# Optimization experiments

Measured on AMD Instinct MI355X. Metric: run time of the kernel, lower is better.

The kernel has to match this reference:

```python
import jax, jax.numpy as jnp
import numpy as np

N = 50000
E = 1600000
AUG = 6
IN = 128
HEADS = 8
HID = 16
OUT = 40


def setup_inputs() -> dict:
    key = jax.random.key(0)
    ks = jax.random.split(key, 14)
    s = 0.1
    return {
        "x": jax.random.normal(ks[0], (N, IN + AUG), jnp.float32),
        "edge_index": jax.random.randint(ks[1], (2, E), 0, N, jnp.int32),
        "mlp_w1": jax.random.normal(ks[2], (AUG, 16), jnp.float32) * s,
        "mlp_b1": jnp.zeros((16,), jnp.float32),
        "mlp_w2": jax.random.normal(ks[3], (16, 1), jnp.float32) * s,
        "mlp_b2": jnp.zeros((1,), jnp.float32),
        "w1": jax.random.normal(ks[4], (IN, HEADS * HID), jnp.float32) * s,
        "att_src1": jax.random.normal(ks[5], (HEADS, HID), jnp.float32) * s,
        "att_dst1": jax.random.normal(ks[6], (HEADS, HID), jnp.float32) * s,
        "bias1": jnp.zeros((HEADS * HID,), jnp.float32),
        "w2": jax.random.normal(ks[7], (HEADS * HID, OUT), jnp.float32) * s,
        "att_src2": jax.random.normal(ks[8], (1, OUT), jnp.float32) * s,
        "att_dst2": jax.random.normal(ks[9], (1, OUT), jnp.float32) * s,
        "bias2": jnp.zeros((OUT,), jnp.float32),
    }


def _gat_conv(x, src, dst, W, att_src, att_dst, bias, concat):
    # PyG GATConv (eval mode): linear -> per-edge leaky_relu attention ->
    # softmax over incoming edges per destination -> weighted scatter-sum.
    n = x.shape[0]
    heads, ch = att_src.shape
    h = (x @ W).reshape(n, heads, ch)                # [N,H,C]
    a_src = (h * att_src[None]).sum(-1)              # [N,H]
    a_dst = (h * att_dst[None]).sum(-1)              # [N,H]
    e = jax.nn.leaky_relu(a_src[src] + a_dst[dst], 0.2)  # [E,H]
    emax = jax.ops.segment_max(e, dst, num_segments=n)   # self-loops ensure nonempty
    p = jnp.exp(e - emax[dst])
    denom = jax.ops.segment_sum(p, dst, num_segments=n)
    alpha = p / denom[dst]                           # [E,H]
    msg = h[src] * alpha[:, :, None]                 # [E,H,C]
    out = jax.ops.segment_sum(msg, dst, num_segments=n)  # [N,H,C]
    out = out.reshape(n, heads * ch) if concat else out.mean(axis=1)
    return out + bias


def reference(x, edge_index, mlp_w1, mlp_b1, mlp_w2, mlp_b2,
              w1, att_src1, att_dst1, bias1, w2, att_src2, att_dst2, bias2):
    n = x.shape[0]
    orig = x[:, :-AUG]
    aug = x[:, -AUG:]
    aug = (aug - aug.mean(axis=0)) / jnp.std(aug, axis=0, ddof=1)  # torch std is unbiased
    scale = jax.nn.sigmoid(jax.nn.relu(aug @ mlp_w1 + mlp_b1) @ mlp_w2 + mlp_b2)  # [N,1]
    h = orig * (1.0 + scale)
    # dropout is identity in eval mode
    loops = jnp.arange(n, dtype=edge_index.dtype)
    src = jnp.concatenate([edge_index[0], loops])
    dst = jnp.concatenate([edge_index[1], loops])
    h = jax.nn.relu(_gat_conv(h, src, dst, w1, att_src1, att_dst1, bias1, True))
    out = _gat_conv(h, src, dst, w2, att_src2, att_dst2, bias2, False)
    return jax.nn.log_softmax(out, axis=1)
```

## Files before the change

kernel.cpp:

```cpp
#include <hip/hip_runtime.h>
#include <hip/hip_fp16.h>

#define XDIM 134
#define FEAT 128
#define AUGN 6
#define NH 8
#define HD 16
#define OUTD 40
#define PS 132
#define SB 256
#define PB 256
#define MAXNB 256
#define G8S 64
#define WTS 130
#define DST 132
#define W2C 48
#define DST2 52

typedef float v2f __attribute__((ext_vector_type(2)));
typedef _Float16 h8t __attribute__((ext_vector_type(8)));
typedef float f32x4 __attribute__((ext_vector_type(4)));

__device__ __forceinline__ float rlf(float v, int lane) {
  return __int_as_float(__builtin_amdgcn_readlane(__float_as_int(v), lane));
}

__global__ __launch_bounds__(256) void k_stats1(const float* __restrict__ x,
                                                float* __restrict__ part,
                                                int N) {
  __shared__ float red[4][12];
  float s[AUGN] = {0, 0, 0, 0, 0, 0}, q[AUGN] = {0, 0, 0, 0, 0, 0};
  for (int n = blockIdx.x * blockDim.x + threadIdx.x; n < N;
       n += gridDim.x * blockDim.x) {
    const float* r = x + (size_t)n * XDIM + FEAT;
    float2 v0 = *(const float2*)r;
    float2 v1 = *(const float2*)(r + 2);
    float2 v2 = *(const float2*)(r + 4);
    float v[AUGN] = {v0.x, v0.y, v1.x, v1.y, v2.x, v2.y};
#pragma unroll
    for (int i = 0; i < AUGN; i++) {
      s[i] += v[i];
      q[i] += v[i] * v[i];
    }
  }
#pragma unroll
  for (int i = 0; i < AUGN; i++) {
    for (int m = 1; m < 64; m <<= 1) {
      s[i] += __shfl_xor(s[i], m);
      q[i] += __shfl_xor(q[i], m);
    }
  }
  int wv = threadIdx.x >> 6, l = threadIdx.x & 63;
  if (l == 0) {
#pragma unroll
    for (int i = 0; i < AUGN; i++) {
      red[wv][i] = s[i];
      red[wv][6 + i] = q[i];
    }
  }
  __syncthreads();
  int t = threadIdx.x;
  if (t < 12) {
    part[blockIdx.x * 12 + t] =
        red[0][t] + red[1][t] + red[2][t] + red[3][t];
  }
}

__global__ __launch_bounds__(256) void k_scale(
    const float* __restrict__ x, const float* __restrict__ part,
    const float* __restrict__ w1, const float* __restrict__ b1,
    const float* __restrict__ w2, const float* __restrict__ b2,
    float* __restrict__ scl, int N) {
  __shared__ float red[4][12];
  __shared__ float sred[12];
  int t = threadIdx.x;
  {
    float v[12];
#pragma unroll
    for (int c = 0; c < 12; c++) v[c] = part[t * 12 + c];
#pragma unroll
    for (int c = 0; c < 12; c++)
      for (int m = 1; m < 64; m <<= 1) v[c] += __shfl_xor(v[c], m);
    int wv = t >> 6, l = t & 63;
    if (l == 0) {
#pragma unroll
      for (int c = 0; c < 12; c++) red[wv][c] = v[c];
    }
    __syncthreads();
    if (t < 12) sred[t] = red[0][t] + red[1][t] + red[2][t] + red[3][t];
    __syncthreads();
  }
  int n = blockIdx.x * 256 + t;
  if (n >= N) return;
  const float* r = x + (size_t)n * XDIM + FEAT;
  float a[AUGN];
  float invN = 1.0f / (float)N;
#pragma unroll
  for (int i = 0; i < AUGN; i++) {
    float sum = sred[i], sq = sred[6 + i];
    float mean = sum * invN;
    float var = (sq - sum * mean) / (float)(N - 1);
    a[i] = (r[i] - mean) / sqrtf(var);
  }
  float s2 = b2[0];
#pragma unroll
  for (int j = 0; j < 16; j++) {
    float z = b1[j];
#pragma unroll
    for (int i = 0; i < AUGN; i++) z = fmaf(a[i], w1[i * 16 + j], z);
    z = fmaxf(z, 0.0f);
    s2 = fmaf(z, w2[j], s2);
  }
  float sig = 1.0f / (1.0f + __expf(-s2));
  scl[n] = 1.0f + sig;
}

__global__ __launch_bounds__(256) void k_bh(const int* __restrict__ ei,
                                            int* __restrict__ cnt, int E,
                                            int NB) {
  __shared__ int hist[MAXNB];
  int t = threadIdx.x;
  for (int b = t; b < NB; b += 256) hist[b] = 0;
  __syncthreads();
  int ch = (E + PB - 1) / PB;
  int lo = blockIdx.x * ch, hi = min(lo + ch, E);
  for (int e = lo + t; e < hi; e += 256)
    atomicAdd(&hist[ei[E + e] >> 8], 1);
  __syncthreads();
  for (int b = t; b < NB; b += 256)
    cnt[(size_t)b * PB + blockIdx.x] = hist[b];
}

__global__ __launch_bounds__(256) void k_sc1(int* __restrict__ cnt,
                                             int* __restrict__ bsum) {
  __shared__ int ps[256];
  int b = blockIdx.x, t = threadIdx.x;
  int v = cnt[(size_t)b * PB + t];
  ps[t] = v;
  __syncthreads();
  for (int d = 1; d < 256; d <<= 1) {
    int u = (t >= d) ? ps[t - d] : 0;
    __syncthreads();
    ps[t] += u;
    __syncthreads();
  }
  cnt[(size_t)b * PB + t] = ps[t] - v;
  if (t == 255) bsum[b] = ps[255];
}

__global__ __launch_bounds__(256) void k_part(const int* __restrict__ ei,
                                              const int* __restrict__ cnt,
                                              const int* __restrict__ bsum,
                                              int* __restrict__ ebuf, int E,
                                              int NB) {
  __shared__ int bex[MAXNB];
  __shared__ int cur[MAXNB];
  int t = threadIdx.x;
  int v = (t < NB) ? bsum[t] : 0;
  bex[t] = v;
  __syncthreads();
  for (int d = 1; d < 256; d <<= 1) {
    int u = (t >= d) ? bex[t - d] : 0;
    __syncthreads();
    bex[t] += u;
    __syncthreads();
  }
  if (t < NB) cur[t] = (bex[t] - v) + cnt[(size_t)t * PB + blockIdx.x];
  __syncthreads();
  int ch = (E + PB - 1) / PB;
  int lo = blockIdx.x * ch, hi = min(lo + ch, E);
  for (int e = lo + t; e < hi; e += 256) {
    int s = ei[e], d = ei[E + e];
    int pos = atomicAdd(&cur[d >> 8], 1);
    ebuf[pos] = (s << 8) | (d & 255);
  }
}

__global__ __launch_bounds__(256) void k_bcsr(const int* __restrict__ ebuf,
                                              const int* __restrict__ bsum,
                                              int* __restrict__ offs,
                                              int* __restrict__ csr, int N,
                                              int E, int NB) {
  __shared__ int bex[MAXNB];
  __shared__ int dl[256];
  __shared__ int sc[256];
  __shared__ int cu[256];
  int b = blockIdx.x, t = threadIdx.x;
  {
    int v = (t < NB) ? bsum[t] : 0;
    bex[t] = v;
    __syncthreads();
    for (int d = 1; d < 256; d <<= 1) {
      int u = (t >= d) ? bex[t - d] : 0;
      __syncthreads();
      bex[t] += u;
      __syncthreads();
    }
    int incl = bex[t];
    __syncthreads();
    bex[t] = incl - v;
    __syncthreads();
  }
  int nn = min(256, N - b * 256);
  int rs = bex[b];
  int re = (b + 1 < NB) ? bex[b + 1] : E;
  int csrbase = rs + b * 256;
  dl[t] = 0;
  __syncthreads();
  for (int j = rs + t; j < re; j += 256)
    atomicAdd(&dl[ebuf[j] & 255], 1);
  __syncthreads();
  int v = (t < nn) ? dl[t] + 1 : 0;
  sc[t] = v;
  __syncthreads();
  for (int d = 1; d < 256; d <<= 1) {
    int u = (t >= d) ? sc[t - d] : 0;
    __syncthreads();
    sc[t] += u;
    __syncthreads();
  }
  int excl = sc[t] - v;
  if (t < nn) {
    int node = b * 256 + t;
    offs[node] = csrbase + excl;
    csr[csrbase + excl] = node;
    cu[t] = excl + 1;
  }
  __syncthreads();
  for (int j = rs + t; j < re; j += 256) {
    int pk = ebuf[j];
    int p = atomicAdd(&cu[pk & 255], 1);
    csr[csrbase + p] = pk >> 8;
  }
  if (b == 0 && t == 0) offs[N] = E + N;
}

__global__ __launch_bounds__(256) void k_gemm1(
    const float* __restrict__ x, const float* __restrict__ scl,
    const float* __restrict__ W, const float* __restrict__ asv,
    const float* __restrict__ adv, unsigned char* __restrict__ h8,
    __half* __restrict__ as1h, __half* __restrict__ ad1h, int N) {
  __shared__ __half WT[128 * WTS];
  __shared__ __half D16[64 * DST];
  int tid = threadIdx.x;
  int wv = tid >> 6, l = tid & 63;
  int q = l >> 4, c = l & 15;
  for (int idx = tid * 4; idx < 128 * 128; idx += 256 * 4) {
    int k = idx >> 7, n = idx & 127;
    float4 v = *(const float4*)(W + idx);
    WT[(n + 0) * WTS + k] = __float2half(v.x);
    WT[(n + 1) * WTS + k] = __float2half(v.y);
    WT[(n + 2) * WTS + k] = __float2half(v.z);
    WT[(n + 3) * WTS + k] = __float2half(v.w);
  }
  __syncthreads();
  int colBase = wv * 32;
  h8t bf[2][4];
  const unsigned short* wtp = (const unsigned short*)WT;
#pragma unroll
  for (int ct = 0; ct < 2; ct++) {
#pragma unroll
    for (int kk = 0; kk < 4; kk++) {
      unsigned int* bu = (unsigned int*)&bf[ct][kk];
      int base = (colBase + ct * 16 + c) * WTS + kk * 32 + 8 * q;
#pragma unroll
      for (int p = 0; p < 4; p++)
        bu[p] = *(const unsigned int*)(wtp + base + 2 * p);
    }
  }
  int nodeBase = blockIdx.x * 64;
#pragma unroll
  for (int nt = 0; nt < 4; nt++) {
    int node = nodeBase + nt * 16 + c;
    const float* xr = x + (size_t)min(node, N - 1) * XDIM;
    h8t af[4];
#pragma unroll
    for (int kk = 0; kk < 4; kk++) {
      int k0 = kk * 32 + 8 * q;
#pragma unroll
      for (int p = 0; p < 4; p++) {
        float2 v = *(const float2*)(xr + k0 + 2 * p);
        af[kk][2 * p] = (_Float16)v.x;
        af[kk][2 * p + 1] = (_Float16)v.y;
      }
    }
    f32x4 a0 = {0.f, 0.f, 0.f, 0.f}, a1 = {0.f, 0.f, 0.f, 0.f};
#pragma unroll
    for (int kk = 0; kk < 4; kk++) {
      a0 = __builtin_amdgcn_mfma_f32_16x16x32_f16(af[kk], bf[0][kk], a0, 0, 0, 0);
      a1 = __builtin_amdgcn_mfma_f32_16x16x32_f16(af[kk], bf[1][kk], a1, 0, 0, 0);
    }
#pragma unroll
    for (int r = 0; r < 4; r++) {
      int row = nt * 16 + 4 * q + r;
      D16[row * DST + colBase + c] = __float2half(a0[r]);
      D16[row * DST + colBase + 16 + c] = __float2half(a1[r]);
    }
  }
  __syncthreads();
  float asw0 = asv[2 * l], asw1 = asv[2 * l + 1];
  float adw0 = adv[2 * l], adw1 = adv[2 * l + 1];
  for (int i = 0; i < 16; i++) {
    int node = nodeBase + wv * 16 + i;
    if (node >= N) break;
    float s = scl[node];
    __half2 yh = *(const __half2*)&D16[(wv * 16 + i) * DST + 2 * l];
    float2 yf = __half22float2(yh);
    float y0 = yf.x * s, y1 = yf.y * s;
    int pk = __builtin_amdgcn_cvt_pk_fp8_f32(y0, y1, 0, false);
    ((unsigned short*)(h8 + (size_t)node * FEAT))[l] = (unsigned short)pk;
    float ps = y0 * asw0 + y1 * asw1;
    float pd = y0 * adw0 + y1 * adw1;
    ps += __shfl_xor(ps, 1); ps += __shfl_xor(ps, 2); ps += __shfl_xor(ps, 4);
    pd += __shfl_xor(pd, 1); pd += __shfl_xor(pd, 2); pd += __shfl_xor(pd, 4);
    if ((l & 7) == 0) {
      as1h[node * NH + (l >> 3)] = __float2half(ps);
      ad1h[node * NH + (l >> 3)] = __float2half(pd);
    }
  }
}

__global__ __launch_bounds__(256) void k_agg1(
    const int* __restrict__ offs, const int* __restrict__ csr,
    const __half* __restrict__ as1h, const __half* __restrict__ ad1h,
    const unsigned char* __restrict__ h8, const float* __restrict__ bias,
    __half* __restrict__ h2h, int N) {
  __shared__ float plds[4][8 * PS];
  __shared__ int slds[4][128];
  int wv = threadIdx.x >> 6, l = threadIdx.x & 63;
  int n = blockIdx.x * 4 + wv;
  if (n >= N) return;
  int beg = offs[n], end = offs[n + 1];
  int deg = end - beg;
  int h = l & 7, e8 = l >> 3;
  float adh = __half2float(ad1h[(size_t)n * NH + h]);
  float smh = 0.0f;
  for (int j0 = 0; j0 < deg; j0 += 8) {
    int j = j0 + e8;
    if (j < deg) {
      int s = csr[beg + j];
      if (h == 0 && j < 128) slds[wv][j] = s;
      float t = __half2float(as1h[(size_t)s * NH + h]) + adh;
      t = t > 0.0f ? t : 0.2f * t;
      float p = __expf(t);
      smh += p;
      if (j < 128) plds[wv][h * PS + j] = p;
    }
  }
  smh += __shfl_xor(smh, 8);
  smh += __shfl_xor(smh, 16);
  smh += __shfl_xor(smh, 32);
  __builtin_amdgcn_wave_barrier();
  int li = l & 15, eg = l >> 4;
  int hh = li >> 1;
  float rd = 1.0f / __shfl(smh, hh);
  const int* sp = slds[wv];
  const float* pp = &plds[wv][hh * PS];
  float acc0 = 0.f, acc1 = 0.f, acc2 = 0.f, acc3 = 0.f;
  float acc4 = 0.f, acc5 = 0.f, acc6 = 0.f, acc7 = 0.f;
  if (deg <= 128) {
    int dm1 = deg - 1;
    int ns = (deg + 3) >> 2;
    uint2 cur[4], nxt[4];
#define ROWA(G) \
  (*(const uint2*)(h8 + (size_t)sp[min(4 * (G) + eg, dm1)] * FEAT + 8 * li))
#pragma unroll
    for (int i = 0; i < 4; i++) cur[i] = ROWA(i);
    for (int g = 0; g < ns; g += 4) {
#pragma unroll
      for (int i = 0; i < 4; i++) nxt[i] = ROWA(g + 4 + i);
#pragma unroll
      for (int i = 0; i < 4; i++) {
        int j = 4 * (g + i) + eg;
        float a = (j < deg) ? pp[j] : 0.0f;
        v2f l0 = __builtin_amdgcn_cvt_pk_f32_fp8((int)cur[i].x, false);
        v2f h0 = __builtin_amdgcn_cvt_pk_f32_fp8((int)cur[i].x, true);
        v2f l1 = __builtin_amdgcn_cvt_pk_f32_fp8((int)cur[i].y, false);
        v2f h1 = __builtin_amdgcn_cvt_pk_f32_fp8((int)cur[i].y, true);
        acc0 = fmaf(a, l0[0], acc0); acc1 = fmaf(a, l0[1], acc1);
        acc2 = fmaf(a, h0[0], acc2); acc3 = fmaf(a, h0[1], acc3);
        acc4 = fmaf(a, l1[0], acc4); acc5 = fmaf(a, l1[1], acc5);
        acc6 = fmaf(a, h1[0], acc6); acc7 = fmaf(a, h1[1], acc7);
        cur[i] = nxt[i];
      }
    }
#undef ROWA
  } else {
    float adhh = __shfl(adh, hh);
    for (int j = eg; j < deg; j += 4) {
      int s;
      float p;
      if (j < 128) {
        s = sp[j];
        p = pp[j];
      } else {
        s = csr[beg + j];
        float t = __half2float(as1h[(size_t)s * NH + hh]) + adhh;
        t = t > 0.0f ? t : 0.2f * t;
        p = __expf(t);
      }
      uint2 w = *(const uint2*)(h8 + (size_t)s * FEAT + 8 * li);
      v2f l0 = __builtin_amdgcn_cvt_pk_f32_fp8((int)w.x, false);
      v2f h0 = __builtin_amdgcn_cvt_pk_f32_fp8((int)w.x, true);
      v2f l1 = __builtin_amdgcn_cvt_pk_f32_fp8((int)w.y, false);
      v2f h1 = __builtin_amdgcn_cvt_pk_f32_fp8((int)w.y, true);
      acc0 = fmaf(p, l0[0], acc0); acc1 = fmaf(p, l0[1], acc1);
      acc2 = fmaf(p, h0[0], acc2); acc3 = fmaf(p, h0[1], acc3);
      acc4 = fmaf(p, l1[0], acc4); acc5 = fmaf(p, l1[1], acc5);
      acc6 = fmaf(p, h1[0], acc6); acc7 = fmaf(p, h1[1], acc7);
    }
  }
#pragma unroll
  for (int m = 16; m < 64; m <<= 1) {
    acc0 += __shfl_xor(acc0, m); acc1 += __shfl_xor(acc1, m);
    acc2 += __shfl_xor(acc2, m); acc3 += __shfl_xor(acc3, m);
    acc4 += __shfl_xor(acc4, m); acc5 += __shfl_xor(acc5, m);
    acc6 += __shfl_xor(acc6, m); acc7 += __shfl_xor(acc7, m);
  }
  if (l < 16) {
    float4 b0 = *(const float4*)(bias + 8 * l);
    float4 b1v = *(const float4*)(bias + 8 * l + 4);
    float o0 = fmaxf(acc0 * rd + b0.x, 0.0f);
    float o1 = fmaxf(acc1 * rd + b0.y, 0.0f);
    float o2 = fmaxf(acc2 * rd + b0.z, 0.0f);
    float o3 = fmaxf(acc3 * rd + b0.w, 0.0f);
    float o4 = fmaxf(acc4 * rd + b1v.x, 0.0f);
    float o5 = fmaxf(acc5 * rd + b1v.y, 0.0f);
    float o6 = fmaxf(acc6 * rd + b1v.z, 0.0f);
    float o7 = fmaxf(acc7 * rd + b1v.w, 0.0f);
    __half2 pa = __float22half2_rn(make_float2(o0, o1));
    __half2 pb = __float22half2_rn(make_float2(o2, o3));
    __half2 pc = __float22half2_rn(make_float2(o4, o5));
    __half2 pd2 = __float22half2_rn(make_float2(o6, o7));
    uint4 st;
    st.x = *(unsigned int*)&pa;
    st.y = *(unsigned int*)&pb;
    st.z = *(unsigned int*)&pc;
    st.w = *(unsigned int*)&pd2;
    *(uint4*)(h2h + (size_t)n * FEAT + 8 * l) = st;
  }
}

__global__ __launch_bounds__(256) void k_gemm2(
    const __half* __restrict__ h2h, const float* __restrict__ W,
    const float* __restrict__ asv, const float* __restrict__ adv,
    unsigned char* __restrict__ g8, float* __restrict__ a_src,
    float* __restrict__ a_dst, int N) {
  __shared__ __half WT2[W2C * WTS];
  __shared__ float DL[64 * DST2];
  int tid = threadIdx.x;
  int wv = tid >> 6, l = tid & 63;
  int q = l >> 4, c = l & 15;
  for (int idx = tid; idx < W2C * 128; idx += 256) {
    int col = idx >> 7, k = idx & 127;
    float v = (col < OUTD) ? W[k * OUTD + col] : 0.0f;
    WT2[col * WTS + k] = __float2half(v);
  }
  __syncthreads();
  h8t bf[3][4];
  const unsigned short* wtp = (const unsigned short*)WT2;
#pragma unroll
  for (int ct = 0; ct < 3; ct++) {
#pragma unroll
    for (int kk = 0; kk < 4; kk++) {
      unsigned int* bu = (unsigned int*)&bf[ct][kk];
      int base = (ct * 16 + c) * WTS + kk * 32 + 8 * q;
#pragma unroll
      for (int p = 0; p < 4; p++)
        bu[p] = *(const unsigned int*)(wtp + base + 2 * p);
    }
  }
  int nodeBase = blockIdx.x * 64;
  int node = nodeBase + wv * 16 + c;
  const __half* hr = h2h + (size_t)min(node, N - 1) * FEAT;
  h8t af[4];
#pragma unroll
  for (int kk = 0; kk < 4; kk++) {
    uint4 v = *(const uint4*)(hr + kk * 32 + 8 * q);
    *(uint4*)&af[kk] = v;
  }
  f32x4 d0 = {0.f, 0.f, 0.f, 0.f}, d1 = {0.f, 0.f, 0.f, 0.f},
        d2 = {0.f, 0.f, 0.f, 0.f};
#pragma unroll
  for (int kk = 0; kk < 4; kk++) {
    d0 = __builtin_amdgcn_mfma_f32_16x16x32_f16(af[kk], bf[0][kk], d0, 0, 0, 0);
    d1 = __builtin_amdgcn_mfma_f32_16x16x32_f16(af[kk], bf[1][kk], d1, 0, 0, 0);
    d2 = __builtin_amdgcn_mfma_f32_16x16x32_f16(af[kk], bf[2][kk], d2, 0, 0, 0);
  }
#pragma unroll
  for (int r = 0; r < 4; r++) {
    int row = wv * 16 + 4 * q + r;
    DL[row * DST2 + c] = d0[r];
    DL[row * DST2 + 16 + c] = d1[r];
    DL[row * DST2 + 32 + c] = d2[r];
  }
  __syncthreads();
  int i = l & 15, cg = l >> 4;
  int row = wv * 16 + i;
  float ps = 0.0f, pd = 0.0f;
#pragma unroll
  for (int k = 0; k < 10; k++) {
    int col = cg * 10 + k;
    float gv = DL[row * DST2 + col];
    ps = fmaf(gv, asv[col], ps);
    pd = fmaf(gv, adv[col], pd);
  }
  ps += __shfl_xor(ps, 16); ps += __shfl_xor(ps, 32);
  pd += __shfl_xor(pd, 16); pd += __shfl_xor(pd, 32);
  int snode = nodeBase + wv * 16 + i;
  if (cg == 0 && snode < N) {
    a_src[snode] = ps;
    a_dst[snode] = pd;
  }
  for (int idx = l; idx < 16 * 16; idx += 64) {
    int ni = idx >> 4, w = idx & 15;
    int rr = wv * 16 + ni;
    int wnode = nodeBase + rr;
    if (wnode < N) {
      unsigned int u = 0;
      if (w < 10) {
        float c0 = DL[rr * DST2 + 4 * w];
        float c1 = DL[rr * DST2 + 4 * w + 1];
        float c2 = DL[rr * DST2 + 4 * w + 2];
        float c3 = DL[rr * DST2 + 4 * w + 3];
        u = __builtin_amdgcn_cvt_pk_fp8_f32(c0, c1, 0, false);
        u = __builtin_amdgcn_cvt_pk_fp8_f32(c2, c3, u, true);
      }
      *(unsigned int*)(g8 + (size_t)wnode * G8S + 4 * w) = u;
    }
  }
}

__global__ __launch_bounds__(256) void k_agg2(
    const int* __restrict__ offs, const int* __restrict__ csr,
    const float* __restrict__ a_src, const float* __restrict__ a_dst,
    const unsigned char* __restrict__ g8, const float* __restrict__ bias,
    float* __restrict__ out, int N) {
  __shared__ float plds[4][PS];
  __shared__ int slds[4][128];
  int wv = threadIdx.x >> 6, l = threadIdx.x & 63;
  int n = blockIdx.x * 4 + wv;
  if (n >= N) return;
  int beg = offs[n], end = offs[n + 1];
  int deg = end - beg;
  float adn = a_dst[n];
  float sm = 0.0f;
  for (int j0 = 0; j0 < deg; j0 += 64) {
    int j = j0 + l;
    if (j < deg) {
      int s = csr[beg + j];
      float t = a_src[s] + adn;
      t = t > 0.0f ? t : 0.2f * t;
      float p = __expf(t);
      sm += p;
      if (j < 128) {
        plds[wv][j] = p;
        slds[wv][j] = s;
      }
    }
  }
  for (int m = 1; m < 64; m <<= 1) sm += __shfl_xor(sm, m);
  float rd = 1.0f / sm;
  const int* sp = slds[wv];
  const float* pp = plds[wv];
  int li = l & 15, eg = l >> 4;
  int lic = min(li, 9);
  const unsigned char* gb = g8 + 4 * lic;
  float acc0 = 0.0f, acc1 = 0.0f, acc2 = 0.0f, acc3 = 0.0f;
  if (deg <= 128) {
    int dm1 = deg - 1;
    int ns = (deg + 3) >> 2;
    unsigned int cur[4], nxt[4];
#define ROWB(G) \
  (*(const unsigned int*)(gb + (size_t)sp[min(4 * (G) + eg, dm1)] * G8S))
#pragma unroll
    for (int i = 0; i < 4; i++) cur[i] = ROWB(i);
    for (int g = 0; g < ns; g += 4) {
#pragma unroll
      for (int i = 0; i < 4; i++) nxt[i] = ROWB(g + 4 + i);
#pragma unroll
      for (int i = 0; i < 4; i++) {
        int j = 4 * (g + i) + eg;
        float a = (j < deg) ? pp[j] : 0.0f;
        v2f lo = __builtin_amdgcn_cvt_pk_f32_fp8((int)cur[i], false);
        v2f hi = __builtin_amdgcn_cvt_pk_f32_fp8((int)cur[i], true);
        acc0 = fmaf(a, lo[0], acc0);
        acc1 = fmaf(a, lo[1], acc1);
        acc2 = fmaf(a, hi[0], acc2);
        acc3 = fmaf(a, hi[1], acc3);
        cur[i] = nxt[i];
      }
    }
#undef ROWB
  } else {
    for (int j = eg; j < deg; j += 4) {
      int s;
      float p;
      if (j < 128) {
        s = sp[j];
        p = pp[j];
      } else {
        s = csr[beg + j];
        float t = a_src[s] + adn;
        t = t > 0.0f ? t : 0.2f * t;
        p = __expf(t);
      }
      unsigned int w = *(const unsigned int*)(gb + (size_t)s * G8S);
      v2f lo = __builtin_amdgcn_cvt_pk_f32_fp8((int)w, false);
      v2f hi = __builtin_amdgcn_cvt_pk_f32_fp8((int)w, true);
      acc0 = fmaf(p, lo[0], acc0);
      acc1 = fmaf(p, lo[1], acc1);
      acc2 = fmaf(p, hi[0], acc2);
      acc3 = fmaf(p, hi[1], acc3);
    }
  }
#pragma unroll
  for (int m = 16; m < 64; m <<= 1) {
    acc0 += __shfl_xor(acc0, m);
    acc1 += __shfl_xor(acc1, m);
    acc2 += __shfl_xor(acc2, m);
    acc3 += __shfl_xor(acc3, m);
  }
  bool cact = li < 10;
  float v0 = -INFINITY, v1 = -INFINITY, v2 = -INFINITY, v3 = -INFINITY;
  if (cact) {
    float4 bv = *(const float4*)(bias + 4 * li);
    v0 = acc0 * rd + bv.x;
    v1 = acc1 * rd + bv.y;
    v2 = acc2 * rd + bv.z;
    v3 = acc3 * rd + bv.w;
  }
  float mx = fmaxf(fmaxf(v0, v1), fmaxf(v2, v3));
  for (int m = 1; m < 64; m <<= 1) mx = fmaxf(mx, __shfl_xor(mx, m));
  float pe = (eg == 0 && cact) ? __expf(v0 - mx) + __expf(v1 - mx) +
                                     __expf(v2 - mx) + __expf(v3 - mx)
                               : 0.0f;
  float se = pe;
  for (int m = 1; m < 64; m <<= 1) se += __shfl_xor(se, m);
  float ls = logf(se);
  if (eg == 0 && cact) {
    float4 o;
    o.x = v0 - mx - ls;
    o.y = v1 - mx - ls;
    o.z = v2 - mx - ls;
    o.w = v3 - mx - ls;
    *(float4*)(out + (size_t)n * OUTD + 4 * li) = o;
  }
}

extern "C" void kernel_launch(void* const* d_in, const int* in_sizes, int n_in,
                              void* d_out, int out_size, void* d_ws,
                              size_t ws_size, hipStream_t stream) {
  const float* x = (const float*)d_in[0];
  const int* ei = (const int*)d_in[1];
  const float* mw1 = (const float*)d_in[2];
  const float* mb1 = (const float*)d_in[3];
  const float* mw2 = (const float*)d_in[4];
  const float* mb2 = (const float*)d_in[5];
  const float* W1 = (const float*)d_in[6];
  const float* as1w = (const float*)d_in[7];
  const float* ad1w = (const float*)d_in[8];
  const float* b1 = (const float*)d_in[9];
  const float* W2 = (const float*)d_in[10];
  const float* as2w = (const float*)d_in[11];
  const float* ad2w = (const float*)d_in[12];
  const float* b2 = (const float*)d_in[13];
  float* out = (float*)d_out;

  int N = in_sizes[0] / XDIM;
  int E = in_sizes[1] / 2;
  int ET = E + N;
  int NB = (N + 255) >> 8;

  char* ws = (char*)d_ws;
  size_t off = 0;
  auto carve = [&](size_t bytes) -> void* {
    void* p = ws + off;
    off = (off + bytes + 255) & ~(size_t)255;
    return p;
  };
  float* part = (float*)carve((size_t)SB * 12 * 4);
  int* cnt = (int*)carve((size_t)NB * PB * 4);
  int* bsum = (int*)carve((size_t)MAXNB * 4);
  int* ebuf = (int*)carve((size_t)E * 4);
  int* offs = (int*)carve((size_t)(N + 1) * 4);
  int* csr = (int*)carve((size_t)ET * 4);
  float* scl = (float*)carve((size_t)N * 4);
  __half* as1h = (__half*)carve((size_t)N * NH * 2);
  __half* ad1h = (__half*)carve((size_t)N * NH * 2);
  unsigned char* h8 = (unsigned char*)carve((size_t)N * FEAT);
  __half* h2h = (__half*)carve((size_t)N * FEAT * 2);
  unsigned char* g8 = (unsigned char*)carve((size_t)N * G8S);
  float* as2 = (float*)carve((size_t)N * 4);
  float* ad2 = (float*)carve((size_t)N * 4);

  k_stats1<<<SB, 256, 0, stream>>>(x, part, N);
  k_scale<<<(N + 255) / 256, 256, 0, stream>>>(x, part, mw1, mb1, mw2, mb2,
                                               scl, N);
  k_bh<<<PB, 256, 0, stream>>>(ei, cnt, E, NB);
  k_sc1<<<NB, 256, 0, stream>>>(cnt, bsum);
  k_part<<<PB, 256, 0, stream>>>(ei, cnt, bsum, ebuf, E, NB);
  k_bcsr<<<NB, 256, 0, stream>>>(ebuf, bsum, offs, csr, N, E, NB);
  int NG = (N + 63) / 64;
  k_gemm1<<<NG, 256, 0, stream>>>(x, scl, W1, as1w, ad1w, h8, as1h, ad1h, N);
  k_agg1<<<(N + 3) / 4, 256, 0, stream>>>(offs, csr, as1h, ad1h, h8, b1, h2h,
                                          N);
  k_gemm2<<<NG, 256, 0, stream>>>(h2h, W2, as2w, ad2w, g8, as2, ad2, N);
  k_agg2<<<(N + 3) / 4, 256, 0, stream>>>(offs, csr, as2, ad2, g8, b2, out, N);
}
```

Before: 182.2 us.

## Merge independent preprocessing kernels into horizontally fused launches

After: 166.7 us. 8.5% less time.

```diff
diff --git a/kernel.cpp b/kernel.cpp
--- a/kernel.cpp
+++ b/kernel.cpp
@@ -25,154 +25,244 @@
   return __int_as_float(__builtin_amdgcn_readlane(__float_as_int(v), lane));
 }
 
-__global__ __launch_bounds__(256) void k_stats1(const float* __restrict__ x,
-                                                float* __restrict__ part,
-                                                int N) {
+__global__ __launch_bounds__(256) void k_f1(const float* __restrict__ x,
+                                            float* __restrict__ part,
+                                            const int* __restrict__ ei,
+                                            int* __restrict__ cnt, int N,
+                                            int E, int NB) {
   __shared__ float red[4][12];
-  float s[AUGN] = {0, 0, 0, 0, 0, 0}, q[AUGN] = {0, 0, 0, 0, 0, 0};
-  for (int n = blockIdx.x * blockDim.x + threadIdx.x; n < N;
-       n += gridDim.x * blockDim.x) {
-    const float* r = x + (size_t)n * XDIM + FEAT;
-    float2 v0 = *(const float2*)r;
-    float2 v1 = *(const float2*)(r + 2);
-    float2 v2 = *(const float2*)(r + 4);
-    float v[AUGN] = {v0.x, v0.y, v1.x, v1.y, v2.x, v2.y};
+  __shared__ int hist[MAXNB];
+  int t = threadIdx.x;
+  if (blockIdx.x < SB) {
+    int bb = blockIdx.x;
+    float s[AUGN] = {0, 0, 0, 0, 0, 0}, q[AUGN] = {0, 0, 0, 0, 0, 0};
+    for (int n = bb * 256 + t; n < N; n += SB * 256) {
+      const float* r = x + (size_t)n * XDIM + FEAT;
+      float2 v0 = *(const float2*)r;
+      float2 v1 = *(const float2*)(r + 2);
+      float2 v2 = *(const float2*)(r + 4);
+      float v[AUGN] = {v0.x, v0.y, v1.x, v1.y, v2.x, v2.y};
+#pragma unroll
+      for (int i = 0; i < AUGN; i++) {
+        s[i] += v[i];
+        q[i] += v[i] * v[i];
+      }
+    }
 #pragma unroll
     for (int i = 0; i < AUGN; i++) {
-      s[i] += v[i];
-      q[i] += v[i] * v[i];
-    }
-  }
-#pragma unroll
-  for (int i = 0; i < AUGN; i++) {
-    for (int m = 1; m < 64; m <<= 1) {
-      s[i] += __shfl_xor(s[i], m);
-      q[i] += __shfl_xor(q[i], m);
-    }
-  }
-  int wv = threadIdx.x >> 6, l = threadIdx.x & 63;
-  if (l == 0) {
-#pragma unroll
-    for (int i = 0; i < AUGN; i++) {
-      red[wv][i] = s[i];
-      red[wv][6 + i] = q[i];
-    }
-  }
-  __syncthreads();
-  int t = threadIdx.x;
-  if (t < 12) {
-    part[blockIdx.x * 12 + t] =
-        red[0][t] + red[1][t] + red[2][t] + red[3][t];
-  }
-}
-
-__global__ __launch_bounds__(256) void k_scale(
+      for (int m = 1; m < 64; m <<= 1) {
+        s[i] += __shfl_xor(s[i], m);
+        q[i] += __shfl_xor(q[i], m);
+      }
+    }
+    int wv = t >> 6, l = t & 63;
+    if (l == 0) {
+#pragma unroll
+      for (int i = 0; i < AUGN; i++) {
+        red[wv][i] = s[i];
+        red[wv][6 + i] = q[i];
+      }
+    }
+    __syncthreads();
+    if (t < 12)
+      part[bb * 12 + t] = red[0][t] + red[1][t] + red[2][t] + red[3][t];
+  } else {
+    int bb = blockIdx.x - SB;
+    for (int b = t; b < NB; b += 256) hist[b] = 0;
+    __syncthreads();
+    int ch = (E + PB - 1) / PB;
+    int lo = bb * ch, hi = min(lo + ch, E);
+    for (int e = lo + t; e < hi; e += 256)
+      atomicAdd(&hist[ei[E + e] >> 8], 1);
+    __syncthreads();
+    for (int b = t; b < NB; b += 256)
+      cnt[(size_t)b * PB + bb] = hist[b];
+  }
+}
+
+__global__ __launch_bounds__(256) void k_f2(
     const float* __restrict__ x, const float* __restrict__ part,
     const float* __restrict__ w1, const float* __restrict__ b1,
     const float* __restrict__ w2, const float* __restrict__ b2,
-    float* __restrict__ scl, int N) {
+    float* __restrict__ scl, int* __restrict__ cnt, int* __restrict__ bsum,
+    int N, int NSC) {
   __shared__ float red[4][12];
   __shared__ float sred[12];
+  __shared__ int ps[256];
   int t = threadIdx.x;
-  {
-    float v[12];
-#pragma unroll
-    for (int c = 0; c < 12; c++) v[c] = part[t * 12 + c];
-#pragma unroll
-    for (int c = 0; c < 12; c++)
-      for (int m = 1; m < 64; m <<= 1) v[c] += __shfl_xor(v[c], m);
-    int wv = t >> 6, l = t & 63;
-    if (l == 0) {
-#pragma unroll
-      for (int c = 0; c < 12; c++) red[wv][c] = v[c];
-    }
-    __syncthreads();
-    if (t < 12) sred[t] = red[0][t] + red[1][t] + red[2][t] + red[3][t];
-    __syncthreads();
-  }
-  int n = blockIdx.x * 256 + t;
-  if (n >= N) return;
-  const float* r = x + (size_t)n * XDIM + FEAT;
-  float a[AUGN];
-  float invN = 1.0f / (float)N;
-#pragma unroll
-  for (int i = 0; i < AUGN; i++) {
-    float sum = sred[i], sq = sred[6 + i];
-    float mean = sum * invN;
-    float var = (sq - sum * mean) / (float)(N - 1);
-    a[i] = (r[i] - mean) / sqrtf(var);
-  }
-  float s2 = b2[0];
-#pragma unroll
-  for (int j = 0; j < 16; j++) {
-    float z = b1[j];
-#pragma unroll
-    for (int i = 0; i < AUGN; i++) z = fmaf(a[i], w1[i * 16 + j], z);
-    z = fmaxf(z, 0.0f);
-    s2 = fmaf(z, w2[j], s2);
-  }
-  float sig = 1.0f / (1.0f + __expf(-s2));
-  scl[n] = 1.0f + sig;
-}
-
-__global__ __launch_bounds__(256) void k_bh(const int* __restrict__ ei,
-                                            int* __restrict__ cnt, int E,
-                                            int NB) {
-  __shared__ int hist[MAXNB];
-  int t = threadIdx.x;
-  for (int b = t; b < NB; b += 256) hist[b] = 0;
-  __syncthreads();
-  int ch = (E + PB - 1) / PB;
-  int lo = blockIdx.x * ch, hi = min(lo + ch, E);
-  for (int e = lo + t; e < hi; e += 256)
-    atomicAdd(&hist[ei[E + e] >> 8], 1);
-  __syncthreads();
-  for (int b = t; b < NB; b += 256)
-    cnt[(size_t)b * PB + blockIdx.x] = hist[b];
-}
-
-__global__ __launch_bounds__(256) void k_sc1(int* __restrict__ cnt,
-                                             int* __restrict__ bsum) {
-  __shared__ int ps[256];
-  int b = blockIdx.x, t = threadIdx.x;
-  int v = cnt[(size_t)b * PB + t];
-  ps[t] = v;
-  __syncthreads();
-  for (int d = 1; d < 256; d <<= 1) {
-    int u = (t >= d) ? ps[t - d] : 0;
-    __syncthreads();
-    ps[t] += u;
-    __syncthreads();
-  }
-  cnt[(size_t)b * PB + t] = ps[t] - v;
-  if (t == 255) bsum[b] = ps[255];
-}
-
-__global__ __launch_bounds__(256) void k_part(const int* __restrict__ ei,
-                                              const int* __restrict__ cnt,
-                                              const int* __restrict__ bsum,
-                                              int* __restrict__ ebuf, int E,
-                                              int NB) {
-  __shared__ int bex[MAXNB];
-  __shared__ int cur[MAXNB];
-  int t = threadIdx.x;
-  int v = (t < NB) ? bsum[t] : 0;
-  bex[t] = v;
-  __syncthreads();
-  for (int d = 1; d < 256; d <<= 1) {
-    int u = (t >= d) ? bex[t - d] : 0;
-    __syncthreads();
-    bex[t] += u;
-    __syncthreads();
-  }
-  if (t < NB) cur[t] = (bex[t] - v) + cnt[(size_t)t * PB + blockIdx.x];
-  __syncthreads();
-  int ch = (E + PB - 1) / PB;
-  int lo = blockIdx.x * ch, hi = min(lo + ch, E);
-  for (int e = lo + t; e < hi; e += 256) {
-    int s = ei[e], d = ei[E + e];
-    int pos = atomicAdd(&cur[d >> 8], 1);
-    ebuf[pos] = (s << 8) | (d & 255);
+  if ((int)blockIdx.x < NSC) {
+    {
+      float v[12];
+#pragma unroll
+      for (int c = 0; c < 12; c++) v[c] = part[t * 12 + c];
+#pragma unroll
+      for (int c = 0; c < 12; c++)
+        for (int m = 1; m < 64; m <<= 1) v[c] += __shfl_xor(v[c], m);
+      int wv = t >> 6, l = t & 63;
+      if (l == 0) {
+#pragma unroll
+        for (int c = 0; c < 12; c++) red[wv][c] = v[c];
+      }
+      __syncthreads();
+      if (t < 12) sred[t] = red[0][t] + red[1][t] + red[2][t] + red[3][t];
+      __syncthreads();
+    }
+    int n = blockIdx.x * 256 + t;
+    if (n >= N) return;
+    const float* r = x + (size_t)n * XDIM + FEAT;
+    float a[AUGN];
+    float invN = 1.0f / (float)N;
+#pragma unroll
+    for (int i = 0; i < AUGN; i++) {
+      float sum = sred[i], sq = sred[6 + i];
+      float mean = sum * invN;
+      float var = (sq - sum * mean) / (float)(N - 1);
+      a[i] = (r[i] - mean) / sqrtf(var);
+    }
+    float s2 = b2[0];
+#pragma unroll
+    for (int j = 0; j < 16; j++) {
+      float z = b1[j];
+#pragma unroll
+      for (int i = 0; i < AUGN; i++) z = fmaf(a[i], w1[i * 16 + j], z);
+      z = fmaxf(z, 0.0f);
+      s2 = fmaf(z, w2[j], s2);
+    }
+    float sig = 1.0f / (1.0f + __expf(-s2));
+    scl[n] = 1.0f + sig;
+  } else {
+    int b = blockIdx.x - NSC;
+    int v = cnt[(size_t)b * PB + t];
+    ps[t] = v;
+    __syncthreads();
+    for (int d = 1; d < 256; d <<= 1) {
+      int u = (t >= d) ? ps[t - d] : 0;
+      __syncthreads();
+      ps[t] += u;
+      __syncthreads();
+    }
+    cnt[(size_t)b * PB + t] = ps[t] - v;
+    if (t == 255) bsum[b] = ps[255];
+  }
+}
+
+__global__ __launch_bounds__(256) void k_f3(
+    const float* __restrict__ x, const float* __restrict__ scl,
+    const float* __restrict__ W, const float* __restrict__ asv,
+    const float* __restrict__ adv, unsigned char* __restrict__ h8,
+    __half* __restrict__ as1h, __half* __restrict__ ad1h,
+    const int* __restrict__ ei, const int* __restrict__ cnt,
+    const int* __restrict__ bsum, int* __restrict__ ebuf, int N, int E,
+    int NB, int NG) {
+  __shared__ __align__(16) char smem[128 * WTS * 2 + 64 * DST * 2];
+  int tid = threadIdx.x;
+  if ((int)blockIdx.x < NG) {
+    __half* WT = (__half*)smem;
+    __half* D16 = (__half*)(smem + 128 * WTS * 2);
+    int wv = tid >> 6, l = tid & 63;
+    int q = l >> 4, c = l & 15;
+    for (int idx = tid * 4; idx < 128 * 128; idx += 256 * 4) {
+      int k = idx >> 7, n = idx & 127;
+      float4 v = *(const float4*)(W + idx);
+      WT[(n + 0) * WTS + k] = __float2half(v.x);
+      WT[(n + 1) * WTS + k] = __float2half(v.y);
+      WT[(n + 2) * WTS + k] = __float2half(v.z);
+      WT[(n + 3) * WTS + k] = __float2half(v.w);
+    }
+    __syncthreads();
+    int colBase = wv * 32;
+    h8t bf[2][4];
+    const unsigned short* wtp = (const unsigned short*)WT;
+#pragma unroll
+    for (int ct = 0; ct < 2; ct++) {
+#pragma unroll
+      for (int kk = 0; kk < 4; kk++) {
+        unsigned int* bu = (unsigned int*)&bf[ct][kk];
+        int base = (colBase + ct * 16 + c) * WTS + kk * 32 + 8 * q;
+#pragma unroll
+        for (int p = 0; p < 4; p++)
+          bu[p] = *(const unsigned int*)(wtp + base + 2 * p);
+      }
+    }
+    int nodeBase = blockIdx.x * 64;
+#pragma unroll
+    for (int nt = 0; nt < 4; nt++) {
+      int node = nodeBase + nt * 16 + c;
+      const float* xr = x + (size_t)min(node, N - 1) * XDIM;
+      h8t af[4];
+#pragma unroll
+      for (int kk = 0; kk < 4; kk++) {
+        int k0 = kk * 32 + 8 * q;
+#pragma unroll
+        for (int p = 0; p < 4; p++) {
+          float2 v = *(const float2*)(xr + k0 + 2 * p);
+          af[kk][2 * p] = (_Float16)v.x;
+          af[kk][2 * p + 1] = (_Float16)v.y;
+        }
+      }
+      f32x4 a0 = {0.f, 0.f, 0.f, 0.f}, a1 = {0.f, 0.f, 0.f, 0.f};
+#pragma unroll
+      for (int kk = 0; kk < 4; kk++) {
+        a0 = __builtin_amdgcn_mfma_f32_16x16x32_f16(af[kk], bf[0][kk], a0, 0,
+                                                    0, 0);
+        a1 = __builtin_amdgcn_mfma_f32_16x16x32_f16(af[kk], bf[1][kk], a1, 0,
+                                                    0, 0);
+      }
+#pragma unroll
+      for (int r = 0; r < 4; r++) {
+        int row = nt * 16 + 4 * q + r;
+        D16[row * DST + colBase + c] = __float2half(a0[r]);
+        D16[row * DST + colBase + 16 + c] = __float2half(a1[r]);
+      }
+    }
+    __syncthreads();
+    float asw0 = asv[2 * l], asw1 = asv[2 * l + 1];
+    float adw0 = adv[2 * l], adw1 = adv[2 * l + 1];
+    for (int i = 0; i < 16; i++) {
+      int node = nodeBase + wv * 16 + i;
+      if (node >= N) break;
+      float s = scl[node];
+      __half2 yh = *(const __half2*)&D16[(wv * 16 + i) * DST + 2 * l];
+      float2 yf = __half22float2(yh);
+      float y0 = yf.x * s, y1 = yf.y * s;
+      int pk = __builtin_amdgcn_cvt_pk_fp8_f32(y0, y1, 0, false);
+      ((unsigned short*)(h8 + (size_t)node * FEAT))[l] = (unsigned short)pk;
+      float ps2 = y0 * asw0 + y1 * asw1;
+      float pd = y0 * adw0 + y1 * adw1;
+      ps2 += __shfl_xor(ps2, 1);
+      ps2 += __shfl_xor(ps2, 2);
+      ps2 += __shfl_xor(ps2, 4);
+      pd += __shfl_xor(pd, 1);
+      pd += __shfl_xor(pd, 2);
+      pd += __shfl_xor(pd, 4);
+      if ((l & 7) == 0) {
+        as1h[node * NH + (l >> 3)] = __float2half(ps2);
+        ad1h[node * NH + (l >> 3)] = __float2half(pd);
+      }
+    }
+  } else {
+    int bb = blockIdx.x - NG;
+    int* bex = (int*)smem;
+    int* cur = (int*)(smem + 1024);
+    int t = tid;
+    int v = (t < NB) ? bsum[t] : 0;
+    bex[t] = v;
+    __syncthreads();
+    for (int d = 1; d < 256; d <<= 1) {
+      int u = (t >= d) ? bex[t - d] : 0;
+      __syncthreads();
+      bex[t] += u;
+      __syncthreads();
+    }
+    if (t < NB) cur[t] = (bex[t] - v) + cnt[(size_t)t * PB + bb];
+    __syncthreads();
+    int ch = (E + PB - 1) / PB;
+    int lo = bb * ch, hi = min(lo + ch, E);
+    for (int e = lo + t; e < hi; e += 256) {
+      int s = ei[e], d = ei[E + e];
+      int pos = atomicAdd(&cur[d >> 8], 1);
+      ebuf[pos] = (s << 8) | (d & 255);
+    }
   }
 }
 
@@ -233,91 +323,6 @@
     csr[csrbase + p] = pk >> 8;
   }
   if (b == 0 && t == 0) offs[N] = E + N;
-}
-
-__global__ __launch_bounds__(256) void k_gemm1(
-    const float* __restrict__ x, const float* __restrict__ scl,
-    const float* __restrict__ W, const float* __restrict__ asv,
-    const float* __restrict__ adv, unsigned char* __restrict__ h8,
-    __half* __restrict__ as1h, __half* __restrict__ ad1h, int N) {
-  __shared__ __half WT[128 * WTS];
-  __shared__ __half D16[64 * DST];
-  int tid = threadIdx.x;
-  int wv = tid >> 6, l = tid & 63;
-  int q = l >> 4, c = l & 15;
-  for (int idx = tid * 4; idx < 128 * 128; idx += 256 * 4) {
-    int k = idx >> 7, n = idx & 127;
-    float4 v = *(const float4*)(W + idx);
-    WT[(n + 0) * WTS + k] = __float2half(v.x);
-    WT[(n + 1) * WTS + k] = __float2half(v.y);
-    WT[(n + 2) * WTS + k] = __float2half(v.z);
-    WT[(n + 3) * WTS + k] = __float2half(v.w);
-  }
-  __syncthreads();
-  int colBase = wv * 32;
-  h8t bf[2][4];
-  const unsigned short* wtp = (const unsigned short*)WT;
-#pragma unroll
-  for (int ct = 0; ct < 2; ct++) {
-#pragma unroll
-    for (int kk = 0; kk < 4; kk++) {
-      unsigned int* bu = (unsigned int*)&bf[ct][kk];
-      int base = (colBase + ct * 16 + c) * WTS + kk * 32 + 8 * q;
-#pragma unroll
-      for (int p = 0; p < 4; p++)
-        bu[p] = *(const unsigned int*)(wtp + base + 2 * p);
-    }
-  }
-  int nodeBase = blockIdx.x * 64;
-#pragma unroll
-  for (int nt = 0; nt < 4; nt++) {
-    int node = nodeBase + nt * 16 + c;
-    const float* xr = x + (size_t)min(node, N - 1) * XDIM;
-    h8t af[4];
-#pragma unroll
-    for (int kk = 0; kk < 4; kk++) {
-      int k0 = kk * 32 + 8 * q;
-#pragma unroll
-      for (int p = 0; p < 4; p++) {
-        float2 v = *(const float2*)(xr + k0 + 2 * p);
-        af[kk][2 * p] = (_Float16)v.x;
-        af[kk][2 * p + 1] = (_Float16)v.y;
-      }
-    }
-    f32x4 a0 = {0.f, 0.f, 0.f, 0.f}, a1 = {0.f, 0.f, 0.f, 0.f};
-#pragma unroll
-    for (int kk = 0; kk < 4; kk++) {
-      a0 = __builtin_amdgcn_mfma_f32_16x16x32_f16(af[kk], bf[0][kk], a0, 0, 0, 0);
-      a1 = __builtin_amdgcn_mfma_f32_16x16x32_f16(af[kk], bf[1][kk], a1, 0, 0, 0);
-    }
-#pragma unroll
-    for (int r = 0; r < 4; r++) {
-      int row = nt * 16 + 4 * q + r;
-      D16[row * DST + colBase + c] = __float2half(a0[r]);
-      D16[row * DST + colBase + 16 + c] = __float2half(a1[r]);
-    }
-  }
-  __syncthreads();
-  float asw0 = asv[2 * l], asw1 = asv[2 * l + 1];
-  float adw0 = adv[2 * l], adw1 = adv[2 * l + 1];
-  for (int i = 0; i < 16; i++) {
-    int node = nodeBase + wv * 16 + i;
-    if (node >= N) break;
-    float s = scl[node];
-    __half2 yh = *(const __half2*)&D16[(wv * 16 + i) * DST + 2 * l];
-    float2 yf = __half22float2(yh);
-    float y0 = yf.x * s, y1 = yf.y * s;
-    int pk = __builtin_amdgcn_cvt_pk_fp8_f32(y0, y1, 0, false);
-    ((unsigned short*)(h8 + (size_t)node * FEAT))[l] = (unsigned short)pk;
-    float ps = y0 * asw0 + y1 * asw1;
-    float pd = y0 * adw0 + y1 * adw1;
-    ps += __shfl_xor(ps, 1); ps += __shfl_xor(ps, 2); ps += __shfl_xor(ps, 4);
-    pd += __shfl_xor(pd, 1); pd += __shfl_xor(pd, 2); pd += __shfl_xor(pd, 4);
-    if ((l & 7) == 0) {
-      as1h[node * NH + (l >> 3)] = __float2half(ps);
-      ad1h[node * NH + (l >> 3)] = __float2half(pd);
-    }
-  }
 }
 
 __global__ __launch_bounds__(256) void k_agg1(
@@ -694,15 +699,14 @@
   float* as2 = (float*)carve((size_t)N * 4);
   float* ad2 = (float*)carve((size_t)N * 4);
 
-  k_stats1<<<SB, 256, 0, stream>>>(x, part, N);
-  k_scale<<<(N + 255) / 256, 256, 0, stream>>>(x, part, mw1, mb1, mw2, mb2,
-                                               scl, N);
-  k_bh<<<PB, 256, 0, stream>>>(ei, cnt, E, NB);
-  k_sc1<<<NB, 256, 0, stream>>>(cnt, bsum);
-  k_part<<<PB, 256, 0, stream>>>(ei, cnt, bsum, ebuf, E, NB);
+  int NSC = (N + 255) / 256;
+  int NG = (N + 63) / 64;
+  k_f1<<<SB + PB, 256, 0, stream>>>(x, part, ei, cnt, N, E, NB);
+  k_f2<<<NSC + NB, 256, 0, stream>>>(x, part, mw1, mb1, mw2, mb2, scl, cnt,
+                                     bsum, N, NSC);
+  k_f3<<<NG + PB, 256, 0, stream>>>(x, scl, W1, as1w, ad1w, h8, as1h, ad1h,
+                                    ei, cnt, bsum, ebuf, N, E, NB, NG);
   k_bcsr<<<NB, 256, 0, stream>>>(ebuf, bsum, offs, csr, N, E, NB);
-  int NG = (N + 63) / 64;
-  k_gemm1<<<NG, 256, 0, stream>>>(x, scl, W1, as1w, ad1w, h8, as1h, ad1h, N);
   k_agg1<<<(N + 3) / 4, 256, 0, stream>>>(offs, csr, as1h, ad1h, h8, b1, h2h,
                                           N);
   k_gemm2<<<NG, 256, 0, stream>>>(h2h, W2, as2w, ad2w, g8, as2, ad2, N);
```
